# Kernel tuning notes

Measured on AMD Instinct MI355X. Metric: run time of the kernel, lower is better.

The kernel has to match this reference:

```python
import jax, jax.numpy as jnp
import numpy as np

V = 100000
E = 524288
D_IN = 128
D_OUT = 128
NUM_REL = 474
BN_EPS = 1e-5


def setup_inputs() -> dict:
    key = jax.random.key(0)
    ks = jax.random.split(key, 12)
    return {
        "x": jax.random.normal(ks[0], (V, D_IN), dtype=jnp.float32),
        "rel_repr": jax.random.normal(ks[1], (NUM_REL, D_IN), dtype=jnp.float32),
        "edge_norm": jax.random.uniform(ks[2], (E,), dtype=jnp.float32),
        "in_w": jax.random.normal(ks[3], (D_IN, D_OUT), dtype=jnp.float32) * 0.1,
        "out_w": jax.random.normal(ks[4], (D_IN, D_OUT), dtype=jnp.float32) * 0.1,
        "loop_w": jax.random.normal(ks[5], (D_IN, D_OUT), dtype=jnp.float32) * 0.1,
        "w_rel": jax.random.normal(ks[6], (D_IN, D_OUT), dtype=jnp.float32) * 0.1,
        "loop_rel": jax.random.normal(ks[7], (1, D_IN), dtype=jnp.float32),
        "bias": jnp.zeros((D_OUT,), dtype=jnp.float32),
        "src": jax.random.randint(ks[8], (E,), 0, V, dtype=jnp.int32),
        "dst": jax.random.randint(ks[9], (E,), 0, V, dtype=jnp.int32),
        "edge_type": jax.random.randint(ks[10], (E,), 0, NUM_REL, dtype=jnp.int32),
    }


def reference(x, rel_repr, edge_norm, in_w, out_w, loop_w, w_rel, loop_rel, bias, src, dst, edge_type):
    # comp primitive 'mult': edge_data = src_emb * rel[edge_type]   [E, D_IN]
    rel = rel_repr  # num_base=-1 -> rel_wt is None, rel.data = rel_repr
    edge_data = x[src] * rel[edge_type]
    half = edge_data.shape[0] // 2  # static under jit
    # first half of edges -> in_w, second half -> out_w
    msg = jnp.concatenate([edge_data[:half] @ in_w, edge_data[half:] @ out_w], axis=0)
    msg = msg * edge_norm[:, None]
    # agg primitive 'sum': scatter-sum into dst nodes
    agg = jax.ops.segment_sum(msg, dst, num_segments=x.shape[0])  # [V, D_OUT]
    # self-loop path: comp(x, loop_rel) @ loop_w
    loop_msg = (x * loop_rel) @ loop_w
    # comb primitive 'add', scaled by 1/3 (dropout with p=0 is identity)
    h = (agg + loop_msg) * (1.0 / 3.0)
    h = h + bias
    # BatchNorm1d, training-mode batch stats, gamma=1, beta=0
    mean = jnp.mean(h, axis=0)
    var = jnp.mean((h - mean) ** 2, axis=0)
    h = (h - mean) * jax.lax.rsqrt(var + BN_EPS)
    # act primitive 'relu'; ltr=True -> project relations
    return jax.nn.relu(h), rel @ w_rel
```

## Files before the change

kernel.cpp:

```cpp
#include <hip/hip_runtime.h>

#define V 100000
#define VP 100096
#define E_EDGES 524288
#define HALF 262144
#define D 128
#define NREL 474
#define BN_EPS 1e-5f
#define NBLK 98

#define ROWTILES 782
#define RED_BLKS 98
#define RELB 237
#define BNBLK 12500

#define LDK 392
#define LDB 40

typedef unsigned short u16;
typedef unsigned int u32;
typedef unsigned long long u64;
typedef __attribute__((ext_vector_type(8))) short short8;
typedef __attribute__((ext_vector_type(4))) float f32x4;

__device__ __forceinline__ u16 f2bf(float f) {
    union { float f; u32 u; } v; v.f = f;
    u32 u = v.u;
    return (u16)((u + 0x7fffu + ((u >> 16) & 1u)) >> 16);
}
__device__ __forceinline__ u32 pk2(float a, float b) {
    return (u32)f2bf(a) | ((u32)f2bf(b) << 16);
}

__global__ __launch_bounds__(256) void hist_k(const int* __restrict__ dst, u32* __restrict__ cnt) {
    int e = blockIdx.x * 256 + threadIdx.x;
    if (e >= E_EDGES) return;
    u32 d = (u32)dst[e];
    if (d >= V) d = 0;
    atomicAdd(&cnt[d], 1u);
}

__global__ __launch_bounds__(1024) void scanA_k(const u32* __restrict__ cnt,
                                                u32* __restrict__ cursor,
                                                u32* __restrict__ bsum) {
    __shared__ u32 wsum[16];
    int tid = threadIdx.x, wid = tid >> 6, lane = tid & 63;
    int idx = blockIdx.x * 1024 + tid;
    u32 v = (idx < V) ? cnt[idx] : 0u;
    u32 s = v;
#pragma unroll
    for (int o = 1; o < 64; o <<= 1) {
        u32 t = __shfl_up(s, o, 64);
        if (lane >= o) s += t;
    }
    if (lane == 63) wsum[wid] = s;
    __syncthreads();
    if (wid == 0) {
        u32 wv = (lane < 16) ? wsum[lane] : 0u;
#pragma unroll
        for (int o = 1; o < 16; o <<= 1) {
            u32 t = __shfl_up(wv, o, 64);
            if (lane >= o) wv += t;
        }
        if (lane < 16) wsum[lane] = wv;
    }
    __syncthreads();
    u32 wprev = wid ? wsum[wid - 1] : 0u;
    if (idx < V) cursor[idx] = s + wprev - v;
    if (tid == 0) bsum[blockIdx.x] = wsum[15];
}

__global__ __launch_bounds__(128) void scanB_k(u32* __restrict__ bsum) {
    __shared__ u32 wtot;
    int t = threadIdx.x, lane = t & 63, w = t >> 6;
    u32 v = (t < NBLK) ? bsum[t] : 0u;
    u32 s = v;
#pragma unroll
    for (int o = 1; o < 64; o <<= 1) {
        u32 x = __shfl_up(s, o, 64);
        if (lane >= o) s += x;
    }
    if (w == 0 && lane == 63) wtot = s;
    __syncthreads();
    u32 add = (w == 1) ? wtot : 0u;
    if (t < NBLK) bsum[t] = add + s - v;
}

__global__ __launch_bounds__(256) void fill_rec_k(
    const int* __restrict__ dst, const int* __restrict__ src, const int* __restrict__ etype,
    const float* __restrict__ enorm, u32* __restrict__ cursor, const u32* __restrict__ bsum,
    u64* __restrict__ rec) {
    int e = blockIdx.x * 256 + threadIdx.x;
    if (e >= E_EDGES) return;
    u32 d = (u32)dst[e];   if (d >= V) d = 0;
    u32 s = (u32)src[e];   if (s >= V) s = 0;
    u32 t = (u32)etype[e]; if (t >= NREL) t = 0;
    float nm = enorm[e];
    u32 w = s | (t << 17) | ((e < HALF ? 0u : 1u) << 26);
    u32 slot = atomicAdd(&cursor[d], 1u) + bsum[d >> 10];
    u64 r = (u64)w | ((u64)__float_as_uint(nm) << 32);
    if (slot < E_EDGES) rec[slot] = r;
}

struct Rec { u32 s, t, hf; float nm; };
__device__ __forceinline__ Rec dec(u64 r) {
    Rec q; u32 w = (u32)r;
    q.s = w & 0x1FFFFu;          if (q.s >= V) q.s = 0;
    q.t = (w >> 17) & 0x1FFu;    if (q.t >= NREL) q.t = 0;
    q.hf = (w >> 26) & 1u;
    q.nm = __uint_as_float((u32)(r >> 32));
    return q;
}

__global__ __launch_bounds__(256) void gather_k(
    const float* __restrict__ x, const float* __restrict__ rel,
    const u32* __restrict__ cursor, const u32* __restrict__ cnt,
    const u32* __restrict__ bsum, const u64* __restrict__ rec, u16* __restrict__ Aagg) {
    int wave = threadIdx.x >> 6, lane = threadIdx.x & 63;
    int v = blockIdx.x * 4 + wave;
    if (v >= VP) return;
    u32* arow = (u32*)(Aagg + (size_t)v * 256);
    if (v >= V) { arow[lane] = 0u; arow[64 + lane] = 0u; return; }

    u32 n = cnt[v];
    u32 end = cursor[v] + bsum[v >> 10];
    if (end > E_EDGES) end = E_EDGES;
    if (n > end) n = end;
    u32 p = end - n;
    int col = lane * 2;

    float iA0 = 0.f, iA1 = 0.f, oA0 = 0.f, oA1 = 0.f;
    float iB0 = 0.f, iB1 = 0.f, oB0 = 0.f, oB1 = 0.f;

    u64 rb0 = 0, rb1 = 0, rb2 = 0, rb3 = 0;
    if (p     < end) rb0 = rec[p];
    if (p + 1 < end) rb1 = rec[p + 1];
    if (p + 2 < end) rb2 = rec[p + 2];
    if (p + 3 < end) rb3 = rec[p + 3];

    for (u32 q = p; q < end; q += 4) {
        u64 rn0 = 0, rn1 = 0, rn2 = 0, rn3 = 0;
        if (q + 4 < end) rn0 = rec[q + 4];
        if (q + 5 < end) rn1 = rec[q + 5];
        if (q + 6 < end) rn2 = rec[q + 6];
        if (q + 7 < end) rn3 = rec[q + 7];

        Rec q0 = dec(rb0), q1 = dec(rb1), q2 = dec(rb2), q3 = dec(rb3);
        float2 x0 = *(const float2*)(x + (size_t)q0.s * D + col);
        float2 x1 = *(const float2*)(x + (size_t)q1.s * D + col);
        float2 x2 = *(const float2*)(x + (size_t)q2.s * D + col);
        float2 x3 = *(const float2*)(x + (size_t)q3.s * D + col);
        float2 v0 = *(const float2*)(rel + (size_t)q0.t * D + col);
        float2 v1 = *(const float2*)(rel + (size_t)q1.t * D + col);
        float2 v2 = *(const float2*)(rel + (size_t)q2.t * D + col);
        float2 v3 = *(const float2*)(rel + (size_t)q3.t * D + col);
        float f00 = x0.x * v0.x * q0.nm, f01 = x0.y * v0.y * q0.nm;
        float f10 = x1.x * v1.x * q1.nm, f11 = x1.y * v1.y * q1.nm;
        float f20 = x2.x * v2.x * q2.nm, f21 = x2.y * v2.y * q2.nm;
        float f30 = x3.x * v3.x * q3.nm, f31 = x3.y * v3.y * q3.nm;
        if (q0.hf) { oA0 += f00; oA1 += f01; } else { iA0 += f00; iA1 += f01; }
        if (q1.hf) { oB0 += f10; oB1 += f11; } else { iB0 += f10; iB1 += f11; }
        if (q2.hf) { oA0 += f20; oA1 += f21; } else { iA0 += f20; iA1 += f21; }
        if (q3.hf) { oB0 += f30; oB1 += f31; } else { iB0 += f30; iB1 += f31; }

        rb0 = rn0; rb1 = rn1; rb2 = rn2; rb3 = rn3;
    }
    arow[lane]      = pk2(iA0 + iB0, iA1 + iB1);
    arow[64 + lane] = pk2(oA0 + oB0, oA1 + oB1);
}

__global__ __launch_bounds__(128) void bt_k(
    const float* __restrict__ in_w, const float* __restrict__ out_w,
    const float* __restrict__ loop_w, u16* __restrict__ Bt) {
    int n = blockIdx.x;
    int t = threadIdx.x;
    const float* Ws[3] = {in_w, out_w, loop_w};
#pragma unroll
    for (int seg = 0; seg < 3; seg++)
        Bt[(size_t)n * 384 + seg * 128 + t] = f2bf(Ws[seg][(size_t)t * D + n]);
}

__global__ __launch_bounds__(512) void gemm_k(
    const u16* __restrict__ Aagg, const u16* __restrict__ Bt,
    const float* __restrict__ x, const float* __restrict__ loop_rel,
    float* __restrict__ h_out, float* __restrict__ psum, float* __restrict__ psq) {
    __shared__ u16 Bs[64 * 384];
    __shared__ float s_sum[64], s_sq[64];
    int tid = threadIdx.x, wave = tid >> 6, lane = tid & 63;
    int half = blockIdx.x & 1;
    int rt   = blockIdx.x >> 1;
    int row0 = rt * 128;

    if (tid < 64) s_sum[tid] = 0.f;
    else if (tid < 128) s_sq[tid - 64] = 0.f;

    int m16 = lane & 15;
    int kq = (lane >> 4) * 8;
    int gvm = row0 + wave * 16 + m16;
    const u16* arow = Aagg + (size_t)gvm * 256;
    bool vok = gvm < V;

    short8 af[8];
#pragma unroll
    for (int ks = 0; ks < 8; ks++) af[ks] = *(const short8*)(arow + ks * 32 + kq);
    float4 xf[8];
    {
        const float* xp = x + (size_t)gvm * D + kq;
#pragma unroll
        for (int kk = 0; kk < 4; kk++) {
            xf[2 * kk]     = vok ? *(const float4*)(xp + kk * 32)     : (float4){0.f, 0.f, 0.f, 0.f};
            xf[2 * kk + 1] = vok ? *(const float4*)(xp + kk * 32 + 4) : (float4){0.f, 0.f, 0.f, 0.f};
        }
    }

    {
        const u16* srcB = Bt + (size_t)half * 64 * 384;
        char* bsb = (char*)Bs;
#pragma unroll
        for (int it = 0; it < 6; it++) {
            int c = it * 512 + tid;
            int n = c / 48, s = c - n * 48;
            short8 vv = *(const short8*)(srcB + (size_t)n * 384 + s * 8);
            *(short8*)(bsb + (((u32)(n * 768 + s * 16)) ^ (u32)((n & 7) << 4))) = vv;
        }
    }
    __syncthreads();

    const char* bsb = (const char*)Bs;
    f32x4 acc[4];
#pragma unroll
    for (int ct = 0; ct < 4; ct++) acc[ct] = (f32x4){0.f, 0.f, 0.f, 0.f};

#pragma unroll
    for (int ks = 0; ks < 8; ks++) {
#pragma unroll
        for (int ct = 0; ct < 4; ct++) {
            int n = ct * 16 + m16;
            short8 b = *(const short8*)(bsb + (((u32)(n * 768 + (ks * 32 + kq) * 2)) ^ (u32)((n & 7) << 4)));
            acc[ct] = __builtin_amdgcn_mfma_f32_16x16x32_bf16(af[ks], b, acc[ct], 0, 0, 0);
        }
    }
#pragma unroll
    for (int kk = 0; kk < 4; kk++) {
        float4 l0 = *(const float4*)(loop_rel + kk * 32 + kq);
        float4 l1 = *(const float4*)(loop_rel + kk * 32 + kq + 4);
        float4 x0 = xf[2 * kk], x1 = xf[2 * kk + 1];
        union { u32 u[4]; short8 s; } c;
        c.u[0] = pk2(x0.x * l0.x, x0.y * l0.y);
        c.u[1] = pk2(x0.z * l0.z, x0.w * l0.w);
        c.u[2] = pk2(x1.x * l1.x, x1.y * l1.y);
        c.u[3] = pk2(x1.z * l1.z, x1.w * l1.w);
#pragma unroll
        for (int ct = 0; ct < 4; ct++) {
            int n = ct * 16 + m16;
            short8 b = *(const short8*)(bsb + (((u32)(n * 768 + (256 + kk * 32 + kq) * 2)) ^ (u32)((n & 7) << 4)));
            acc[ct] = __builtin_amdgcn_mfma_f32_16x16x32_bf16(c.s, b, acc[ct], 0, 0, 0);
        }
    }

    int m4 = (lane >> 4) * 4;
#pragma unroll
    for (int ct = 0; ct < 4; ct++) {
        float ls = 0.f, lq = 0.f;
#pragma unroll
        for (int i = 0; i < 4; i++) {
            int gv = row0 + wave * 16 + m4 + i;
            if (gv < V) {
                float h = acc[ct][i] * (1.0f / 3.0f);
                h_out[(size_t)gv * D + half * 64 + ct * 16 + m16] = h;
                ls += h; lq += h * h;
            }
        }
        atomicAdd(&s_sum[ct * 16 + m16], ls);
        atomicAdd(&s_sq[ct * 16 + m16], lq);
    }
    __syncthreads();
    if (tid < 64) psum[(size_t)rt * 128 + half * 64 + tid] = s_sum[tid];
    else if (tid < 128) psq[(size_t)rt * 128 + half * 64 + (tid - 64)] = s_sq[tid - 64];
}

__global__ __launch_bounds__(256) void bn_reduce(
    const float* __restrict__ psum, const float* __restrict__ psq,
    float* __restrict__ colsum, float* __restrict__ colsumsq) {
    int t = threadIdx.x;
    int c = t & 127;
    const float* srcp = (t < 128) ? psum : psq;
    float s = 0.f;
    int r0 = blockIdx.x * 8;
#pragma unroll
    for (int i = 0; i < 8; i++) {
        int r = r0 + i;
        if (r < ROWTILES) s += srcp[(size_t)r * 128 + c];
    }
    atomicAdd(((t < 128) ? colsum : colsumsq) + c, s);
}

__global__ __launch_bounds__(256) void final_k(
    float* __restrict__ hio, const float* __restrict__ colsum, const float* __restrict__ colsumsq,
    const float* __restrict__ rel, const float* __restrict__ w, float* __restrict__ out1) {
    int bid = blockIdx.x;
    if (bid < RELB) {
        __shared__ float rs[2][D];
        int rh = threadIdx.x >> 7, c = threadIdx.x & 127;
        int r = bid * 2 + rh;
        rs[rh][c] = rel[(size_t)r * D + c];
        __syncthreads();
        float s = 0.f;
#pragma unroll 8
        for (int k = 0; k < D; k++) s += rs[rh][k] * w[(size_t)k * D + c];
        out1[(size_t)r * D + c] = s;
        return;
    }
    int idx = ((bid - RELB) * 256 + threadIdx.x) * 4;
    if (idx >= V * D) return;
    int col = idx & (D - 1);
    float4 hv = *(const float4*)(hio + idx);
    float4 ov;
    {
        float m0 = colsum[col + 0] * (1.0f / (float)V);
        float m1 = colsum[col + 1] * (1.0f / (float)V);
        float m2 = colsum[col + 2] * (1.0f / (float)V);
        float m3 = colsum[col + 3] * (1.0f / (float)V);
        if (!isfinite(m0)) m0 = 0.f;
        if (!isfinite(m1)) m1 = 0.f;
        if (!isfinite(m2)) m2 = 0.f;
        if (!isfinite(m3)) m3 = 0.f;
        float v0 = colsumsq[col + 0] * (1.0f / (float)V) - m0 * m0;
        float v1 = colsumsq[col + 1] * (1.0f / (float)V) - m1 * m1;
        float v2 = colsumsq[col + 2] * (1.0f / (float)V) - m2 * m2;
        float v3 = colsumsq[col + 3] * (1.0f / (float)V) - m3 * m3;
        if (!isfinite(v0) || v0 < 0.f) v0 = 0.f;
        if (!isfinite(v1) || v1 < 0.f) v1 = 0.f;
        if (!isfinite(v2) || v2 < 0.f) v2 = 0.f;
        if (!isfinite(v3) || v3 < 0.f) v3 = 0.f;
        float f0 = (hv.x - m0) * rsqrtf(v0 + BN_EPS);
        float f1 = (hv.y - m1) * rsqrtf(v1 + BN_EPS);
        float f2 = (hv.z - m2) * rsqrtf(v2 + BN_EPS);
        float f3 = (hv.w - m3) * rsqrtf(v3 + BN_EPS);
        ov.x = (f0 > 0.f) ? f0 : 0.f;
        ov.y = (f1 > 0.f) ? f1 : 0.f;
        ov.z = (f2 > 0.f) ? f2 : 0.f;
        ov.w = (f3 > 0.f) ? f3 : 0.f;
    }
    *(float4*)(hio + idx) = ov;
}

__global__ __launch_bounds__(1024) void scan_k(const u32* __restrict__ cnt,
                                               u32* __restrict__ cursor) {
    __shared__ u32 wsum[16];
    __shared__ u32 carry_s;
    int tid = threadIdx.x, wid = tid >> 6, lane = tid & 63;
    if (tid == 0) carry_s = 0;
    __syncthreads();
    for (int base = 0; base < V; base += 1024) {
        int idx = base + tid;
        u32 v = (idx < V) ? cnt[idx] : 0u;
        u32 s = v;
#pragma unroll
        for (int o = 1; o < 64; o <<= 1) {
            u32 t = __shfl_up(s, o, 64);
            if (lane >= o) s += t;
        }
        if (lane == 63) wsum[wid] = s;
        __syncthreads();
        if (wid == 0) {
            u32 wv = (lane < 16) ? wsum[lane] : 0u;
#pragma unroll
            for (int o = 1; o < 16; o <<= 1) {
                u32 t = __shfl_up(wv, o, 64);
                if (lane >= o) wv += t;
            }
            if (lane < 16) wsum[lane] = wv;
        }
        __syncthreads();
        u32 wprev = (wid == 0) ? 0u : wsum[wid - 1];
        u32 c = carry_s;
        if (idx < V) cursor[idx] = c + s + wprev - v;
        u32 tot = wsum[15];
        __syncthreads();
        if (tid == 0) carry_s = c + tot;
        __syncthreads();
    }
}

__global__ __launch_bounds__(256) void fill_k(
    const int* __restrict__ dst, u32* __restrict__ cursor, u32* __restrict__ eid) {
    int e = blockIdx.x * 256 + threadIdx.x;
    if (e >= E_EDGES) return;
    u32 d = (u32)dst[e];
    if (d >= V) d = 0;
    u32 slot = atomicAdd(&cursor[d], 1u);
    if (slot < E_EDGES) eid[slot] = (u32)e;
}

__global__ __launch_bounds__(256, 1) void fused_k(
    const float* __restrict__ x, const float* __restrict__ rel, const float* __restrict__ loop_rel,
    const float* __restrict__ in_w, const float* __restrict__ out_w, const float* __restrict__ loop_w,
    const float* __restrict__ enorm,
    const int* __restrict__ src, const int* __restrict__ etype,
    const u32* __restrict__ cursor, const u32* __restrict__ cnt,
    const u32* __restrict__ eid,
    float* __restrict__ h_out, float* __restrict__ colsum, float* __restrict__ colsumsq) {
    __shared__ u16 Alds[64 * LDK];
    __shared__ u16 Bs[D * LDB];
    __shared__ float s_sum[D], s_sq[D];

    int tid = threadIdx.x, wave = tid >> 6, lane = tid & 63;
    int row0 = blockIdx.x * 64;

    if (tid < D) { s_sum[tid] = 0.f; s_sq[tid] = 0.f; }

    for (int i = 0; i < 16; i++) {
        int row = wave * 16 + i;
        int gv = row0 + row;
        u32* arow = (u32*)(Alds + row * LDK);
        if (gv < V) {
            float a0 = 0.f, a1 = 0.f, b0 = 0.f, b1 = 0.f;
            float c0 = 0.f, c1 = 0.f, d0 = 0.f, d1 = 0.f;
            u32 n = cnt[gv];
            u32 end = cursor[gv];
            u32 beg = (end >= n) ? end - n : 0u;
            if (beg >= E_EDGES) { beg = 0; n = 0; }
            if (n > E_EDGES - beg) n = E_EDGES - beg;
            u32 nend = beg + n;
            u32 p = beg;
            for (; p + 2 <= nend; p += 2) {
                u32 e0 = eid[p];           if (e0 >= E_EDGES) e0 = 0;
                u32 e1 = eid[p + 1];       if (e1 >= E_EDGES) e1 = 0;
                u32 s0 = (u32)src[e0];     if (s0 >= V) s0 = 0;
                u32 s1 = (u32)src[e1];     if (s1 >= V) s1 = 0;
                u32 t0 = (u32)etype[e0];   if (t0 >= NREL) t0 = 0;
                u32 t1 = (u32)etype[e1];   if (t1 >= NREL) t1 = 0;
                float n0 = enorm[e0];
                float n1 = enorm[e1];
                float2 xv0 = *(const float2*)(x + (size_t)s0 * D + lane * 2);
                float2 xv1 = *(const float2*)(x + (size_t)s1 * D + lane * 2);
                float2 rv0 = *(const float2*)(rel + (size_t)t0 * D + lane * 2);
                float2 rv1 = *(const float2*)(rel + (size_t)t1 * D + lane * 2);
                float f00 = xv0.x * rv0.x * n0, f01 = xv0.y * rv0.y * n0;
                float f10 = xv1.x * rv1.x * n1, f11 = xv1.y * rv1.y * n1;
                if (e0 < HALF) { a0 += f00; a1 += f01; } else { b0 += f00; b1 += f01; }
                if (e1 < HALF) { c0 += f10; c1 += f11; } else { d0 += f10; d1 += f11; }
            }
            if (p < nend) {
                u32 e0 = eid[p];           if (e0 >= E_EDGES) e0 = 0;
                u32 s0 = (u32)src[e0];     if (s0 >= V) s0 = 0;
                u32 t0 = (u32)etype[e0];   if (t0 >= NREL) t0 = 0;
                float n0 = enorm[e0];
                float2 xv0 = *(const float2*)(x + (size_t)s0 * D + lane * 2);
                float2 rv0 = *(const float2*)(rel + (size_t)t0 * D + lane * 2);
                float f00 = xv0.x * rv0.x * n0, f01 = xv0.y * rv0.y * n0;
                if (e0 < HALF) { a0 += f00; a1 += f01; } else { b0 += f00; b1 += f01; }
            }
            a0 += c0; a1 += c1; b0 += d0; b1 += d1;
            float2 xv = *(const float2*)(x + (size_t)gv * D + lane * 2);
            float2 lv = *(const float2*)(loop_rel + lane * 2);
            arow[lane]       = pk2(a0, a1);
            arow[64 + lane]  = pk2(b0, b1);
            arow[128 + lane] = pk2(xv.x * lv.x, xv.y * lv.y);
        } else {
            arow[lane] = 0u; arow[64 + lane] = 0u; arow[128 + lane] = 0u;
        }
    }
    __syncthreads();

    f32x4 acc[8];
#pragma unroll
    for (int ct = 0; ct < 8; ct++) acc[ct] = (f32x4){0.f, 0.f, 0.f, 0.f};

    int m = wave * 16 + (lane & 15);
    int kq = (lane >> 4) * 8;
    int bk = tid >> 3;
    int bn0 = (tid & 7) * 16;

    for (int ks = 0; ks < 12; ks++) {
        int k0 = ks * 32;
        int seg = k0 >> 7;
        int kloc = k0 & 127;
        const float* W = (seg == 0) ? in_w : (seg == 1 ? out_w : loop_w);
#pragma unroll
        for (int j = 0; j < 16; j += 2) {
            float2 w2 = *(const float2*)(W + (size_t)(kloc + bk) * D + bn0 + j);
            Bs[(bn0 + j) * LDB + bk]     = f2bf(w2.x);
            Bs[(bn0 + j + 1) * LDB + bk] = f2bf(w2.y);
        }
        __syncthreads();
        short8 a = *(const short8*)(Alds + m * LDK + k0 + kq);
#pragma unroll
        for (int ct = 0; ct < 8; ct++) {
            short8 b = *(const short8*)(Bs + (ct * 16 + (lane & 15)) * LDB + kq);
            acc[ct] = __builtin_amdgcn_mfma_f32_16x16x32_bf16(a, b, acc[ct], 0, 0, 0);
        }
        __syncthreads();
    }

    int m4 = (lane >> 4) * 4;
#pragma unroll
    for (int ct = 0; ct < 8; ct++) {
        float ls = 0.f, lq = 0.f;
#pragma unroll
        for (int i = 0; i < 4; i++) {
            int gv = row0 + wave * 16 + m4 + i;
            if (gv < V) {
                float h = acc[ct][i] * (1.0f / 3.0f);
                h_out[(size_t)gv * D + ct * 16 + (lane & 15)] = h;
                ls += h; lq += h * h;
            }
        }
        atomicAdd(&s_sum[ct * 16 + (lane & 15)], ls);
        atomicAdd(&s_sq[ct * 16 + (lane & 15)], lq);
    }
    __syncthreads();
    if (tid < D) atomicAdd(&colsum[tid], s_sum[tid]);
    else atomicAdd(&colsumsq[tid - D], s_sq[tid - D]);
}

__global__ void bn_finalize(const float* __restrict__ colsum, const float* __restrict__ colsumsq,
                            float* __restrict__ mean, float* __restrict__ scale) {
    int t = threadIdx.x;
    float m = colsum[t] * (1.0f / (float)V);
    if (!isfinite(m)) m = 0.f;
    float var = colsumsq[t] * (1.0f / (float)V) - m * m;
    if (!isfinite(var) || var < 0.f) var = 0.f;
    mean[t] = m;
    scale[t] = rsqrtf(var + BN_EPS);
}

__global__ __launch_bounds__(256) void bn_relu(
    float* __restrict__ hio, const float* __restrict__ mean, const float* __restrict__ scale) {
    int idx = (blockIdx.x * 256 + threadIdx.x) * 4;
    if (idx >= V * D) return;
    int col = idx & (D - 1);
    float4 hv = *(const float4*)(hio + idx);
    float f0 = (hv.x - mean[col + 0]) * scale[col + 0];
    float f1 = (hv.y - mean[col + 1]) * scale[col + 1];
    float f2 = (hv.z - mean[col + 2]) * scale[col + 2];
    float f3 = (hv.w - mean[col + 3]) * scale[col + 3];
    f0 = (f0 > 0.f) ? f0 : 0.f;
    f1 = (f1 > 0.f) ? f1 : 0.f;
    f2 = (f2 > 0.f) ? f2 : 0.f;
    f3 = (f3 > 0.f) ? f3 : 0.f;
    float4 ov; ov.x = f0; ov.y = f1; ov.z = f2; ov.w = f3;
    *(float4*)(hio + idx) = ov;
}

__global__ __launch_bounds__(128) void rel_gemm(
    const float* __restrict__ rel, const float* __restrict__ w, float* __restrict__ out1) {
    __shared__ float rs[D];
    int t = threadIdx.x;
    int r = blockIdx.x;
    rs[t] = rel[(size_t)r * D + t];
    __syncthreads();
    float s = 0.f;
#pragma unroll 8
    for (int k = 0; k < D; k++) s += rs[k] * w[(size_t)k * D + t];
    out1[(size_t)r * D + t] = s;
}

extern "C" void kernel_launch(void* const* d_in, const int* in_sizes, int n_in,
                              void* d_out, int out_size, void* d_ws, size_t ws_size,
                              hipStream_t stream) {
    const float* x        = (const float*)d_in[0];
    const float* rel_repr = (const float*)d_in[1];
    const float* enorm    = (const float*)d_in[2];
    const float* in_w     = (const float*)d_in[3];
    const float* out_w    = (const float*)d_in[4];
    const float* loop_w   = (const float*)d_in[5];
    const float* w_rel    = (const float*)d_in[6];
    const float* loop_rel = (const float*)d_in[7];
    const int* src   = (const int*)d_in[9];
    const int* dst   = (const int*)d_in[10];
    const int* etype = (const int*)d_in[11];

    float* out0 = (float*)d_out;
    float* out1 = (float*)d_out + (size_t)V * D;

    char* ws = (char*)d_ws;

    {
        size_t off = 0;
        u32* cnt        = (u32*)(ws + off); off += (size_t)V * 4;
        float* colsum   = (float*)(ws + off); off += 512;
        float* colsumsq = (float*)(ws + off); off += 512;
        size_t zero_bytes = off;
        u32* cursor = (u32*)(ws + off); off += (size_t)V * 4;
        u32* bsum   = (u32*)(ws + off); off += 512;
        u16* Bt     = (u16*)(ws + off); off += (size_t)128 * 384 * 2;
        float* psum = (float*)(ws + off); off += (size_t)ROWTILES * 128 * 4;
        float* psq  = (float*)(ws + off); off += (size_t)ROWTILES * 128 * 4;
        u64* rec    = (u64*)(ws + off); off += (size_t)E_EDGES * 8;
        u16* Aagg   = (u16*)(ws + off); off += (size_t)VP * 256 * 2;

        if (ws_size >= off) {
            hipMemsetAsync(d_ws, 0, zero_bytes, stream);
            bt_k<<<128, 128, 0, stream>>>(in_w, out_w, loop_w, Bt);
            hist_k<<<(E_EDGES + 255) / 256, 256, 0, stream>>>(dst, cnt);
            scanA_k<<<NBLK, 1024, 0, stream>>>(cnt, cursor, bsum);
            scanB_k<<<1, 128, 0, stream>>>(bsum);
            fill_rec_k<<<(E_EDGES + 255) / 256, 256, 0, stream>>>(dst, src, etype, enorm, cursor, bsum, rec);
            gather_k<<<VP / 4, 256, 0, stream>>>(x, rel_repr, cursor, cnt, bsum, rec, Aagg);
            gemm_k<<<ROWTILES * 2, 512, 0, stream>>>(Aagg, Bt, x, loop_rel, out0, psum, psq);
            bn_reduce<<<RED_BLKS, 256, 0, stream>>>(psum, psq, colsum, colsumsq);
            final_k<<<RELB + BNBLK, 256, 0, stream>>>(out0, colsum, colsumsq, rel_repr, w_rel, out1);
            return;
        }
    }

    {
        size_t off = 0;
        u32* cnt      = (u32*)(ws + off); off += (size_t)V * 4;
        float* colsum = (float*)(ws + off); off += 512;
        float* colsumsq = (float*)(ws + off); off += 512;
        size_t zero_bytes = off;
        u32* cursor   = (u32*)(ws + off); off += (size_t)V * 4;
        float* meanp  = (float*)(ws + off); off += 512;
        float* scalep = (float*)(ws + off); off += 512;
        u32* eid      = (u32*)(ws + off); off += (size_t)E_EDGES * 4;

        if (ws_size < off) return;

        hipMemsetAsync(d_ws, 0, zero_bytes, stream);
        hist_k<<<(E_EDGES + 255) / 256, 256, 0, stream>>>(dst, cnt);
        scan_k<<<1, 1024, 0, stream>>>(cnt, cursor);
        fill_k<<<(E_EDGES + 255) / 256, 256, 0, stream>>>(dst, cursor, eid);
        fused_k<<<(V + 63) / 64, 256, 0, stream>>>(x, rel_repr, loop_rel, in_w, out_w, loop_w,
                                                   enorm, src, etype,
                                                   cursor, cnt, eid,
                                                   out0, colsum, colsumsq);
        bn_finalize<<<1, 128, 0, stream>>>(colsum, colsumsq, meanp, scalep);
        bn_relu<<<(V * D / 4 + 255) / 256, 256, 0, stream>>>(out0, meanp, scalep);
        rel_gemm<<<NREL, 128, 0, stream>>>(rel_repr, w_rel, out1);
    }
}
```

Before: 335.1 us.

## Fuse weight transpose into scan kernel, merge GEMM column halves, simplify gather loop

The bf16 weight transpose kernel is folded into the single-block scan kernel as extra blocks, which removes one launch. The GEMM now has each block compute both 64-column halves in turn, reloading the B tile into shared memory for each half. This halves the grid and avoids reading the A rows and x twice, at the cost of more accumulator registers and a serial B reload. The gather loop drops its software-prefetched record pipeline in favour of a plain unrolled-by-4 loop with a scalar tail.

```diff
diff --git a/kernel.cpp b/kernel.cpp
--- a/kernel.cpp
+++ b/kernel.cpp
@@ -70,7 +70,19 @@
     if (tid == 0) bsum[blockIdx.x] = wsum[15];
 }
 
-__global__ __launch_bounds__(128) void scanB_k(u32* __restrict__ bsum) {
+__global__ __launch_bounds__(128) void scanBbt_k(
+    u32* __restrict__ bsum,
+    const float* __restrict__ in_w, const float* __restrict__ out_w,
+    const float* __restrict__ loop_w, u16* __restrict__ Bt) {
+    if (blockIdx.x > 0) {
+        int n = blockIdx.x - 1;
+        int t = threadIdx.x;
+        const float* Ws[3] = {in_w, out_w, loop_w};
+#pragma unroll
+        for (int seg = 0; seg < 3; seg++)
+            Bt[(size_t)n * 384 + seg * 128 + t] = f2bf(Ws[seg][(size_t)t * D + n]);
+        return;
+    }
     __shared__ u32 wtot;
     int t = threadIdx.x, lane = t & 63, w = t >> 6;
     u32 v = (t < NBLK) ? bsum[t] : 0u;
@@ -118,7 +130,6 @@
     const u32* __restrict__ bsum, const u64* __restrict__ rec, u16* __restrict__ Aagg) {
     int wave = threadIdx.x >> 6, lane = threadIdx.x & 63;
     int v = blockIdx.x * 4 + wave;
-    if (v >= VP) return;
     u32* arow = (u32*)(Aagg + (size_t)v * 256);
     if (v >= V) { arow[lane] = 0u; arow[64 + lane] = 0u; return; }
 
@@ -132,20 +143,9 @@
     float iA0 = 0.f, iA1 = 0.f, oA0 = 0.f, oA1 = 0.f;
     float iB0 = 0.f, iB1 = 0.f, oB0 = 0.f, oB1 = 0.f;
 
-    u64 rb0 = 0, rb1 = 0, rb2 = 0, rb3 = 0;
-    if (p     < end) rb0 = rec[p];
-    if (p + 1 < end) rb1 = rec[p + 1];
-    if (p + 2 < end) rb2 = rec[p + 2];
-    if (p + 3 < end) rb3 = rec[p + 3];
-
-    for (u32 q = p; q < end; q += 4) {
-        u64 rn0 = 0, rn1 = 0, rn2 = 0, rn3 = 0;
-        if (q + 4 < end) rn0 = rec[q + 4];
-        if (q + 5 < end) rn1 = rec[q + 5];
-        if (q + 6 < end) rn2 = rec[q + 6];
-        if (q + 7 < end) rn3 = rec[q + 7];
-
-        Rec q0 = dec(rb0), q1 = dec(rb1), q2 = dec(rb2), q3 = dec(rb3);
+    for (; p + 4 <= end; p += 4) {
+        u64 r0 = rec[p], r1 = rec[p + 1], r2 = rec[p + 2], r3 = rec[p + 3];
+        Rec q0 = dec(r0), q1 = dec(r1), q2 = dec(r2), q3 = dec(r3);
         float2 x0 = *(const float2*)(x + (size_t)q0.s * D + col);
         float2 x1 = *(const float2*)(x + (size_t)q1.s * D + col);
         float2 x2 = *(const float2*)(x + (size_t)q2.s * D + col);
@@ -162,22 +162,17 @@
         if (q1.hf) { oB0 += f10; oB1 += f11; } else { iB0 += f10; iB1 += f11; }
         if (q2.hf) { oA0 += f20; oA1 += f21; } else { iA0 += f20; iA1 += f21; }
         if (q3.hf) { oB0 += f30; oB1 += f31; } else { iB0 += f30; iB1 += f31; }
-
-        rb0 = rn0; rb1 = rn1; rb2 = rn2; rb3 = rn3;
+    }
+    for (; p < end; p++) {
+        u64 r0 = rec[p];
+        Rec q0 = dec(r0);
+        float2 x0 = *(const float2*)(x + (size_t)q0.s * D + col);
+        float2 v0 = *(const float2*)(rel + (size_t)q0.t * D + col);
+        float f00 = x0.x * v0.x * q0.nm, f01 = x0.y * v0.y * q0.nm;
+        if (q0.hf) { oA0 += f00; oA1 += f01; } else { iA0 += f00; iA1 += f01; }
     }
     arow[lane]      = pk2(iA0 + iB0, iA1 + iB1);
     arow[64 + lane] = pk2(oA0 + oB0, oA1 + oB1);
-}
-
-__global__ __launch_bounds__(128) void bt_k(
-    const float* __restrict__ in_w, const float* __restrict__ out_w,
-    const float* __restrict__ loop_w, u16* __restrict__ Bt) {
-    int n = blockIdx.x;
-    int t = threadIdx.x;
-    const float* Ws[3] = {in_w, out_w, loop_w};
-#pragma unroll
-    for (int seg = 0; seg < 3; seg++)
-        Bt[(size_t)n * 384 + seg * 128 + t] = f2bf(Ws[seg][(size_t)t * D + n]);
 }
 
 __global__ __launch_bounds__(512) void gemm_k(
@@ -185,14 +180,13 @@
     const float* __restrict__ x, const float* __restrict__ loop_rel,
     float* __restrict__ h_out, float* __restrict__ psum, float* __restrict__ psq) {
     __shared__ u16 Bs[64 * 384];
-    __shared__ float s_sum[64], s_sq[64];
+    __shared__ float s_sum[D], s_sq[D];
     int tid = threadIdx.x, wave = tid >> 6, lane = tid & 63;
-    int half = blockIdx.x & 1;
-    int rt   = blockIdx.x >> 1;
+    int rt = blockIdx.x;
     int row0 = rt * 128;
 
-    if (tid < 64) s_sum[tid] = 0.f;
-    else if (tid < 128) s_sq[tid - 64] = 0.f;
+    if (tid < D) s_sum[tid] = 0.f;
+    else if (tid < 2 * D) s_sq[tid - D] = 0.f;
 
     int m16 = lane & 15;
     int kq = (lane >> 4) * 8;
@@ -203,19 +197,32 @@
     short8 af[8];
 #pragma unroll
     for (int ks = 0; ks < 8; ks++) af[ks] = *(const short8*)(arow + ks * 32 + kq);
-    float4 xf[8];
+    short8 lf[4];
     {
         const float* xp = x + (size_t)gvm * D + kq;
 #pragma unroll
         for (int kk = 0; kk < 4; kk++) {
-            xf[2 * kk]     = vok ? *(const float4*)(xp + kk * 32)     : (float4){0.f, 0.f, 0.f, 0.f};
-            xf[2 * kk + 1] = vok ? *(const float4*)(xp + kk * 32 + 4) : (float4){0.f, 0.f, 0.f, 0.f};
-        }
-    }
-
-    {
-        const u16* srcB = Bt + (size_t)half * 64 * 384;
-        char* bsb = (char*)Bs;
+            float4 x0 = vok ? *(const float4*)(xp + kk * 32)     : (float4){0.f, 0.f, 0.f, 0.f};
+            float4 x1 = vok ? *(const float4*)(xp + kk * 32 + 4) : (float4){0.f, 0.f, 0.f, 0.f};
+            float4 l0 = *(const float4*)(loop_rel + kk * 32 + kq);
+            float4 l1 = *(const float4*)(loop_rel + kk * 32 + kq + 4);
+            union { u32 u[4]; short8 s; } c;
+            c.u[0] = pk2(x0.x * l0.x, x0.y * l0.y);
+            c.u[1] = pk2(x0.z * l0.z, x0.w * l0.w);
+            c.u[2] = pk2(x1.x * l1.x, x1.y * l1.y);
+            c.u[3] = pk2(x1.z * l1.z, x1.w * l1.w);
+            lf[kk] = c.s;
+        }
+    }
+
+    f32x4 acc[8];
+#pragma unroll
+    for (int i = 0; i < 8; i++) acc[i] = (f32x4){0.f, 0.f, 0.f, 0.f};
+
+    char* bsb = (char*)Bs;
+#pragma unroll
+    for (int h = 0; h < 2; h++) {
+        const u16* srcB = Bt + (size_t)h * 64 * 384;
 #pragma unroll
         for (int it = 0; it < 6; it++) {
             int c = it * 512 + tid;
@@ -223,60 +230,52 @@
             short8 vv = *(const short8*)(srcB + (size_t)n * 384 + s * 8);
             *(short8*)(bsb + (((u32)(n * 768 + s * 16)) ^ (u32)((n & 7) << 4))) = vv;
         }
-    }
-    __syncthreads();
-
-    const char* bsb = (const char*)Bs;
-    f32x4 acc[4];
-#pragma unroll
-    for (int ct = 0; ct < 4; ct++) acc[ct] = (f32x4){0.f, 0.f, 0.f, 0.f};
-
-#pragma unroll
-    for (int ks = 0; ks < 8; ks++) {
+        __syncthreads();
+
+#pragma unroll
+        for (int ks = 0; ks < 8; ks++) {
+#pragma unroll
+            for (int ct = 0; ct < 4; ct++) {
+                int n = ct * 16 + m16;
+                short8 b = *(const short8*)(bsb + (((u32)(n * 768 + (ks * 32 + kq) * 2)) ^ (u32)((n & 7) << 4)));
+                acc[h * 4 + ct] = __builtin_amdgcn_mfma_f32_16x16x32_bf16(af[ks], b, acc[h * 4 + ct], 0, 0, 0);
+            }
+        }
+#pragma unroll
+        for (int kk = 0; kk < 4; kk++) {
+#pragma unroll
+            for (int ct = 0; ct < 4; ct++) {
+                int n = ct * 16 + m16;
+                short8 b = *(const short8*)(bsb + (((u32)(n * 768 + (256 + kk * 32 + kq) * 2)) ^ (u32)((n & 7) << 4)));
+                acc[h * 4 + ct] = __builtin_amdgcn_mfma_f32_16x16x32_bf16(lf[kk], b, acc[h * 4 + ct], 0, 0, 0);
+            }
+        }
+        __syncthreads();
+    }
+
+    int m4 = (lane >> 4) * 4;
+#pragma unroll
+    for (int h = 0; h < 2; h++) {
 #pragma unroll
         for (int ct = 0; ct < 4; ct++) {
-            int n = ct * 16 + m16;
-            short8 b = *(const short8*)(bsb + (((u32)(n * 768 + (ks * 32 + kq) * 2)) ^ (u32)((n & 7) << 4)));
-            acc[ct] = __builtin_amdgcn_mfma_f32_16x16x32_bf16(af[ks], b, acc[ct], 0, 0, 0);
-        }
-    }
-#pragma unroll
-    for (int kk = 0; kk < 4; kk++) {
-        float4 l0 = *(const float4*)(loop_rel + kk * 32 + kq);
-        float4 l1 = *(const float4*)(loop_rel + kk * 32 + kq + 4);
-        float4 x0 = xf[2 * kk], x1 = xf[2 * kk + 1];
-        union { u32 u[4]; short8 s; } c;
-        c.u[0] = pk2(x0.x * l0.x, x0.y * l0.y);
-        c.u[1] = pk2(x0.z * l0.z, x0.w * l0.w);
-        c.u[2] = pk2(x1.x * l1.x, x1.y * l1.y);
-        c.u[3] = pk2(x1.z * l1.z, x1.w * l1.w);
-#pragma unroll
-        for (int ct = 0; ct < 4; ct++) {
-            int n = ct * 16 + m16;
-            short8 b = *(const short8*)(bsb + (((u32)(n * 768 + (256 + kk * 32 + kq) * 2)) ^ (u32)((n & 7) << 4)));
-            acc[ct] = __builtin_amdgcn_mfma_f32_16x16x32_bf16(c.s, b, acc[ct], 0, 0, 0);
-        }
-    }
-
-    int m4 = (lane >> 4) * 4;
-#pragma unroll
-    for (int ct = 0; ct < 4; ct++) {
-        float ls = 0.f, lq = 0.f;
-#pragma unroll
-        for (int i = 0; i < 4; i++) {
-            int gv = row0 + wave * 16 + m4 + i;
-            if (gv < V) {
-                float h = acc[ct][i] * (1.0f / 3.0f);
-                h_out[(size_t)gv * D + half * 64 + ct * 16 + m16] = h;
-                ls += h; lq += h * h;
+            float ls = 0.f, lq = 0.f;
+            f32x4 a = acc[h * 4 + ct];
+#pragma unroll
+            for (int i = 0; i < 4; i++) {
+                int gv = row0 + wave * 16 + m4 + i;
+                if (gv < V) {
+                    float hx = a[i] * (1.0f / 3.0f);
+                    h_out[(size_t)gv * D + h * 64 + ct * 16 + m16] = hx;
+                    ls += hx; lq += hx * hx;
+                }
             }
-        }
-        atomicAdd(&s_sum[ct * 16 + m16], ls);
-        atomicAdd(&s_sq[ct * 16 + m16], lq);
-    }
-    __syncthreads();
-    if (tid < 64) psum[(size_t)rt * 128 + half * 64 + tid] = s_sum[tid];
-    else if (tid < 128) psq[(size_t)rt * 128 + half * 64 + (tid - 64)] = s_sq[tid - 64];
+            atomicAdd(&s_sum[h * 64 + ct * 16 + m16], ls);
+            atomicAdd(&s_sq[h * 64 + ct * 16 + m16], lq);
+        }
+    }
+    __syncthreads();
+    if (tid < D) psum[(size_t)rt * 128 + tid] = s_sum[tid];
+    else if (tid < 2 * D) psq[(size_t)rt * 128 + (tid - D)] = s_sq[tid - D];
 }
 
 __global__ __launch_bounds__(256) void bn_reduce(
@@ -593,13 +592,12 @@
 
         if (ws_size >= off) {
             hipMemsetAsync(d_ws, 0, zero_bytes, stream);
-            bt_k<<<128, 128, 0, stream>>>(in_w, out_w, loop_w, Bt);
             hist_k<<<(E_EDGES + 255) / 256, 256, 0, stream>>>(dst, cnt);
             scanA_k<<<NBLK, 1024, 0, stream>>>(cnt, cursor, bsum);
-            scanB_k<<<1, 128, 0, stream>>>(bsum);
+            scanBbt_k<<<129, 128, 0, stream>>>(bsum, in_w, out_w, loop_w, Bt);
             fill_rec_k<<<(E_EDGES + 255) / 256, 256, 0, stream>>>(dst, src, etype, enorm, cursor, bsum, rec);
             gather_k<<<VP / 4, 256, 0, stream>>>(x, rel_repr, cursor, cnt, bsum, rec, Aagg);
-            gemm_k<<<ROWTILES * 2, 512, 0, stream>>>(Aagg, Bt, x, loop_rel, out0, psum, psq);
+            gemm_k<<<ROWTILES, 512, 0, stream>>>(Aagg, Bt, x, loop_rel, out0, psum, psq);
             bn_reduce<<<RED_BLKS, 256, 0, stream>>>(psum, psq, colsum, colsumsq);
             final_k<<<RELB + BNBLK, 256, 0, stream>>>(out0, colsum, colsumsq, rel_repr, w_rel, out1);
             return;
```

Measured after the change: 341.8 us. Within noise of the previous version (+2.0%).
